# Performance work log

Measured on AMD Instinct MI355X. Metric: run time of the kernel, lower is better.

The kernel has to match this reference:

```python
import jax, jax.numpy as jnp
import numpy as np

B, C, T, H = 2, 1024, 2048, 16
D = C // H  # head dim = 64
SCALE = 1.0 / np.sqrt(D)
NEG_INF = jnp.float32(-1e30)


def setup_inputs() -> dict:
    key = jax.random.key(0)
    ks = jax.random.split(key, 10)
    x = jax.random.normal(ks[0], (B, C, T), dtype=jnp.float32)
    mask = jax.random.randint(ks[1], (B, 1, T), 0, 2).astype(bool)
    mask = mask.at[:, :, 0].set(True)  # avoid all-masked rows -> NaN softmax
    w = 1.0 / np.sqrt(C)
    Wq = jax.random.normal(ks[2], (C, C), dtype=jnp.float32) * w
    bq = jax.random.normal(ks[3], (C,), dtype=jnp.float32) * 0.01
    Wk = jax.random.normal(ks[4], (C, C), dtype=jnp.float32) * w
    bk = jax.random.normal(ks[5], (C,), dtype=jnp.float32) * 0.01
    Wv = jax.random.normal(ks[6], (C, C), dtype=jnp.float32) * w
    bv = jax.random.normal(ks[7], (C,), dtype=jnp.float32) * 0.01
    Wp = jax.random.normal(ks[8], (C, C), dtype=jnp.float32) * w
    bp = jax.random.normal(ks[9], (C,), dtype=jnp.float32) * 0.01
    return {"x": x, "mask": mask, "Wq": Wq, "bq": bq, "Wk": Wk, "bk": bk,
            "Wv": Wv, "bv": bv, "Wp": Wp, "bp": bp}


def _proj(W, b, x):
    # Conv1d with kernel_size=1: per-timestep linear on [B, C, T]
    return jnp.einsum('oc,bct->bot', W, x) + b[:, None]


def _heads(y):
    # [B, C, T] -> [B, H, T, D]
    return y.reshape(B, H, D, T).transpose(0, 1, 3, 2)


def reference(x, mask, Wq, bq, Wk, bk, Wv, bv, Wp, bp):
    q = _heads(_proj(Wq, bq, x))  # [B,H,T,D]
    k = _heads(_proj(Wk, bk, x))
    v = _heads(_proj(Wv, bv, x))
    att = jnp.einsum('bhqd,bhkd->bhqk', q * SCALE, k)  # [B,H,T,T]
    att = jnp.where(mask[:, :, None, :], att, NEG_INF)  # mask keys
    att = jax.nn.softmax(att, axis=-1)
    vm = v * mask[:, :, :, None].astype(v.dtype)  # zero masked values
    out = jnp.einsum('bhqk,bhkd->bhqd', att, vm)  # [B,H,T,D]
    out = out.transpose(0, 1, 3, 2).reshape(B, C, T)
    out = _proj(Wp, bp, out) * mask.astype(x.dtype)  # [B,C,T]
    return (out, mask)
```

## Files before the change

kernel.cpp:

```cpp
#include <hip/hip_runtime.h>
#include <hip/hip_bf16.h>
#include <math.h>

#define BB 2
#define CC 1024
#define TT 2048
#define HH 16
#define DD 64

using short8   = __attribute__((ext_vector_type(8))) short;
using floatx4  = __attribute__((ext_vector_type(4))) float;
using floatx16 = __attribute__((ext_vector_type(16))) float;
using uint2v   = __attribute__((ext_vector_type(2))) unsigned int;
typedef unsigned short ushort_t;

#define MFMA(a, b, c) __builtin_amdgcn_mfma_f32_16x16x32_bf16((a), (b), (c), 0, 0, 0)
#define MFMA32(a, b, c) __builtin_amdgcn_mfma_f32_32x32x16_bf16((a), (b), (c), 0, 0, 0)

#define QSC 0.18033688011112042f

#define PMAGIC   8404857.0f
#define PZERO_BF 0.97265625f

__device__ __forceinline__ ushort_t f2bf(float f) {
    unsigned int u = __float_as_uint(f);
    u += 0x7FFFu + ((u >> 16) & 1u);
    return (ushort_t)(u >> 16);
}
__device__ __forceinline__ float bf2f(ushort_t h) {
    return __uint_as_float(((unsigned int)h) << 16);
}
__device__ __forceinline__ ushort_t f2bf_t(float f) {
    return (ushort_t)(__float_as_uint(f) >> 16);
}
__device__ __forceinline__ unsigned int packtrunc(float a, float b) {
    return __builtin_amdgcn_perm(__float_as_uint(b), __float_as_uint(a),
                                 0x07060302u);
}
__device__ __forceinline__ unsigned int pack2bf_exp(float s0, float s1) {
    float f0 = fmaf(s0, 128.0f, PMAGIC);
    float f1 = fmaf(s1, 128.0f, PMAGIC);
    return __builtin_amdgcn_perm(__float_as_uint(f1), __float_as_uint(f0),
                                 0x05040100u);
}
__device__ __forceinline__ void load_lds16(const void* g, void* s) {
    __builtin_amdgcn_global_load_lds(
        (const __attribute__((address_space(1))) void*)g,
        (__attribute__((address_space(3))) void*)s, 16, 0, 0);
}

static constexpr size_t B0       = 65536;
static constexpr size_t XT_OFF   = B0;
static constexpr size_t WQKV_OFF = XT_OFF   + 8388608;
static constexpr size_t WP_OFF   = WQKV_OFF + 6291456;
static constexpr size_t Q_OFF    = WP_OFF   + 2097152;
static constexpr size_t K_OFF    = Q_OFF    + 8388608;
static constexpr size_t V_OFF    = K_OFF    + 8388608;
static constexpr size_t OP_OFF   = V_OFF    + 8388608;
static constexpr size_t ML_OFF   = OP_OFF   + 16777216;

__global__ __launch_bounds__(256) void prep_kernel(
    const float* __restrict__ x, const float* __restrict__ Wq,
    const float* __restrict__ Wk, const float* __restrict__ Wv,
    const float* __restrict__ Wp, const unsigned int* __restrict__ mraw,
    ushort_t* __restrict__ XT, ushort_t* __restrict__ WQKV,
    ushort_t* __restrict__ WP, float* __restrict__ maskf,
    int* __restrict__ nmcnt, float* __restrict__ out_tail) {
    __shared__ float tile[64][65];
    const int bid = blockIdx.x;
    const int tid = threadIdx.x;
    if (bid < 4096) {
        const int idx = bid * 256 + tid;
        if (idx < 786432) {
            int row = idx >> 8;
            int qc  = idx & 255;
            const float* src = row < 1024 ? Wq : (row < 2048 ? Wk : Wv);
            float4 v = *(const float4*)&src[(size_t)(row & 1023) * CC + qc * 4];
            ushort4 pk; pk.x = f2bf(v.x); pk.y = f2bf(v.y);
            pk.z = f2bf(v.z); pk.w = f2bf(v.w);
            *(ushort4*)&WQKV[(size_t)idx * 4] = pk;
        } else {
            int j = idx - 786432;
            float4 v = *(const float4*)&Wp[(size_t)j * 4];
            ushort4 pk; pk.x = f2bf(v.x); pk.y = f2bf(v.y);
            pk.z = f2bf(v.z); pk.w = f2bf(v.w);
            *(ushort4*)&WP[(size_t)j * 4] = pk;
        }
    } else if (bid < 5120) {
        const int xb = bid - 4096;
        const int t0 = (xb & 31) * 64, c0 = ((xb >> 5) & 15) * 64, b = xb >> 9;
        const int tc = tid & 15, tr = tid >> 4;
        #pragma unroll
        for (int p = 0; p < 4; p++) {
            int cl = tr + p * 16;
            float4 v = *(const float4*)&x[((size_t)b * CC + c0 + cl) * TT + t0 + tc * 4];
            tile[cl][tc * 4 + 0] = v.x; tile[cl][tc * 4 + 1] = v.y;
            tile[cl][tc * 4 + 2] = v.z; tile[cl][tc * 4 + 3] = v.w;
        }
        __syncthreads();
        #pragma unroll
        for (int p = 0; p < 4; p++) {
            int tl = tr + p * 16;
            ushort4 pk;
            pk.x = f2bf(tile[tc * 4 + 0][tl]);
            pk.y = f2bf(tile[tc * 4 + 1][tl]);
            pk.z = f2bf(tile[tc * 4 + 2][tl]);
            pk.w = f2bf(tile[tc * 4 + 3][tl]);
            *(ushort4*)&XT[((size_t)b * TT + t0 + tl) * CC + c0 + tc * 4] = pk;
        }
    } else {
        __shared__ int ev_bf16, ev_bool, cnt;
        const int mb = bid - 5120;
        if (tid == 0) { ev_bf16 = 0; ev_bool = 0; cnt = 0; }
        __syncthreads();
        for (int i = tid; i < 1024; i += 256) {
            unsigned int w = mraw[i];
            if ((w & 0xFFFFu) == 0x3F80u) atomicOr(&ev_bf16, 1);
            if ((w & 0xFFFFFF00u) != 0u && w != 0x3F800000u) atomicOr(&ev_bool, 1);
        }
        __syncthreads();
        const int mode = ev_bf16 ? 2 : (ev_bool ? 1 : 0);
        const int e = mb * 256 + tid;
        bool on;
        if (mode == 2)      on = ((const ushort_t*)mraw)[e] != 0;
        else if (mode == 1) on = ((const unsigned char*)mraw)[e] != 0;
        else                on = mraw[e] != 0;
        maskf[e]    = on ? 1.0f : 0.0f;
        out_tail[e] = on ? 1.0f : 0.0f;
        if (!on) atomicAdd(&cnt, 1);
        __syncthreads();
        if (tid == 0) nmcnt[mb] = cnt;
    }
}

__global__ __launch_bounds__(256) void gemm_qkv_kernel(
    const ushort_t* __restrict__ Wqkv, const float* __restrict__ bq,
    const float* __restrict__ bk, const float* __restrict__ bv,
    const ushort_t* __restrict__ XT, const float* __restrict__ maskf,
    ushort_t* __restrict__ Qo, ushort_t* __restrict__ Ko,
    ushort_t* __restrict__ Vo) {
    __shared__ ushort_t As[128][32];
    __shared__ ushort_t Bs[128][32];
    __shared__ float biasS[128];

    const int b = blockIdx.z;
    const int m0 = blockIdx.y * 128;
    const int n0 = blockIdx.x * 128;
    const int tid = threadIdx.x;
    const int lane = tid & 63;
    const int w = tid >> 6;
    const int wm = (w & 1) * 64, wn = (w >> 1) * 64;
    const int la = lane & 15, lg = lane >> 4;
    const int region = m0 >> 10;

    const float* bsrc = region == 0 ? (bq + m0)
                      : (region == 1 ? (bk + m0 - 1024) : (bv + m0 - 2048));
    if (tid < 128) biasS[tid] = bsrc[tid];

    float csc[4];
    #pragma unroll
    for (int nt = 0; nt < 4; nt++) {
        const int t = n0 + wn + nt * 16 + la;
        csc[nt] = (region == 0) ? QSC : maskf[b * TT + t];
    }

    floatx4 zero4 = {0.f, 0.f, 0.f, 0.f};
    floatx4 acc[4][4];
    #pragma unroll
    for (int mt = 0; mt < 4; mt++)
        #pragma unroll
        for (int nt = 0; nt < 4; nt++) acc[mt][nt] = zero4;

    const ushort_t* Abase = Wqkv + (size_t)m0 * CC;
    const ushort_t* Bbase = XT + ((size_t)b * TT + n0) * CC;
    const int rl = lane >> 2;
    const int cl = (lane & 3) * 8;

    for (int k0 = 0; k0 < CC; k0 += 32) {
        #pragma unroll
        for (int c = 0; c < 2; c++) {
            int row = w * 32 + c * 16;
            load_lds16(Abase + (size_t)(row + rl) * CC + k0 + cl, &As[row][0]);
            load_lds16(Bbase + (size_t)(row + rl) * CC + k0 + cl, &Bs[row][0]);
        }
        __syncthreads();
        short8 af[4], bf[4];
        #pragma unroll
        for (int mt = 0; mt < 4; mt++)
            af[mt] = *(const short8*)&As[wm + mt * 16 + la][lg * 8];
        #pragma unroll
        for (int nt = 0; nt < 4; nt++)
            bf[nt] = *(const short8*)&Bs[wn + nt * 16 + la][lg * 8];
        #pragma unroll
        for (int mt = 0; mt < 4; mt++)
            #pragma unroll
            for (int nt = 0; nt < 4; nt++)
                acc[mt][nt] = MFMA(af[mt], bf[nt], acc[mt][nt]);
        __syncthreads();
    }

    #pragma unroll
    for (int mt = 0; mt < 4; mt++) {
        const int lm = wm + mt * 16 + lg * 4;
        const int gm = m0 + lm;
        #pragma unroll
        for (int nt = 0; nt < 4; nt++) {
            const int t = n0 + wn + nt * 16 + la;
            const float sc = csc[nt];
            float v0 = (acc[mt][nt][0] + biasS[lm + 0]) * sc;
            float v1 = (acc[mt][nt][1] + biasS[lm + 1]) * sc;
            float v2 = (acc[mt][nt][2] + biasS[lm + 2]) * sc;
            float v3 = (acc[mt][nt][3] + biasS[lm + 3]) * sc;
            if (region < 2) {
                int mq = gm & 1023;
                int hh = mq >> 6, db = mq & 63;
                ushort_t* dst = (region == 0 ? Qo : Ko)
                              + (((size_t)b * HH + hh) * TT + t) * DD + db;
                uint2 pk;
                pk.x = packtrunc(v0, v1);
                pk.y = packtrunc(v2, v3);
                *(uint2*)dst = pk;
            } else {
                int c = gm & 1023;
                Vo[((size_t)b * CC + c + 0) * TT + t] = f2bf_t(v0);
                Vo[((size_t)b * CC + c + 1) * TT + t] = f2bf_t(v1);
                Vo[((size_t)b * CC + c + 2) * TT + t] = f2bf_t(v2);
                Vo[((size_t)b * CC + c + 3) * TT + t] = f2bf_t(v3);
            }
        }
    }
}

__global__ __launch_bounds__(256, 4) void attn_kernel(
    const ushort_t* __restrict__ Qg, const ushort_t* __restrict__ Kg,
    const ushort_t* __restrict__ Vg, const int* __restrict__ nmcnt,
    ushort_t* __restrict__ Opart, float* __restrict__ lbuf) {
    __shared__ __align__(16) char ldsbuf[32768];

    const unsigned int bid = blockIdx.x;
    const unsigned int xcd = bid & 7u;
    const unsigned int rr  = bid >> 3;
    const unsigned int x   = rr & 15u;
    const unsigned int j   = rr >> 4;
    const unsigned int g   = (j << 3) | xcd;
    const int hh  = (int)(g & 15u);
    const int z   = (int)(g >> 4);
    const int sp  = z & 1, b = z >> 1;
    const int t0  = (int)x * 128;

    const int j0base = sp * (TT / 2);
    const int tid  = threadIdx.x;
    const int lane = tid & 63;
    const int w    = tid >> 6;
    const int ln31 = lane & 31;
    const int h    = lane >> 5;
    const size_t qkbase = ((size_t)b * HH + hh) * TT * DD;
    const size_t vbase  = ((size_t)b * CC + hh * DD) * TT;

    const int tq = t0 + w * 32 + ln31;
    short8 qreg[4];
    {
        const ushort_t* qp = Qg + qkbase + (size_t)tq * DD + h * 8;
        #pragma unroll
        for (int kc = 0; kc < 4; kc++)
            qreg[kc] = *(const short8*)(qp + kc * 16);
    }

    const int i3   = lane >> 3;
    const int swzb = (((lane & 7) + 8 - i3) & 7) << 4;
    const char* ks0 = (const char*)(Kg + qkbase + (size_t)(j0base + 16 * w + i3) * DD) + swzb;
    const char* vs0 = (const char*)(Vg + vbase + (size_t)(16 * w + i3) * TT + j0base) + swzb;
    char* kd = ldsbuf + 2 * w * 1024;
    char* vd = ldsbuf + 16384 + 2 * w * 1024;

    int ka[4];
    #pragma unroll
    for (int kc = 0; kc < 4; kc++)
        ka[kc] = ln31 * 128 + (((kc * 2 + h + ln31) & 7) << 4);

    floatx16 zero16 = {0.f,0.f,0.f,0.f,0.f,0.f,0.f,0.f,
                       0.f,0.f,0.f,0.f,0.f,0.f,0.f,0.f};
    floatx16 oacc[2];
    oacc[0] = zero16; oacc[1] = zero16;
    floatx16 lacc = zero16;
    short8 ones8;
    #pragma unroll
    for (int i = 0; i < 8; i++) ones8[i] = (short)0x3F80;

    load_lds16(ks0,          kd);
    load_lds16(ks0 + 1024,   kd + 1024);
    load_lds16(vs0,          vd);
    load_lds16(vs0 + 32768,  vd + 1024);
    ks0 += 8192; vs0 += 128;
    __syncthreads();

    #pragma unroll 2
    for (int kt = 0; kt < 16; kt++) {
        const int pp = (kt & 1) * 8192;
        const int pn = 8192 - pp;
        if (kt < 15) {
            load_lds16(ks0,         kd + pn);
            load_lds16(ks0 + 1024,  kd + pn + 1024);
            load_lds16(vs0,         vd + pn);
            load_lds16(vs0 + 32768, vd + pn + 1024);
            ks0 += 8192; vs0 += 128;
        }

        floatx16 sacc[2];
        sacc[0] = zero16; sacc[1] = zero16;
        __builtin_amdgcn_s_setprio(1);
        #pragma unroll
        for (int kc = 0; kc < 4; kc++) {
            short8 kf0 = *(const short8*)(ldsbuf + ka[kc] + pp);
            short8 kf1 = *(const short8*)(ldsbuf + ka[kc] + pp + 4096);
            sacc[0] = MFMA32(kf0, qreg[kc], sacc[0]);
            sacc[1] = MFMA32(kf1, qreg[kc], sacc[1]);
        }
        __builtin_amdgcn_s_setprio(0);

        unsigned int pd[16];
        #pragma unroll
        for (int mt = 0; mt < 2; mt++)
            #pragma unroll
            for (int g2 = 0; g2 < 4; g2++) {
                pd[mt * 8 + g2 * 2 + 0] =
                    pack2bf_exp(sacc[mt][g2 * 4 + 0], sacc[mt][g2 * 4 + 1]);
                pd[mt * 8 + g2 * 2 + 1] =
                    pack2bf_exp(sacc[mt][g2 * 4 + 2], sacc[mt][g2 * 4 + 3]);
            }

        __builtin_amdgcn_s_setprio(1);
        #pragma unroll
        for (int kc = 0; kc < 4; kc++) {
            const int base = (kc >> 1) * 8 + (kc & 1) * 4;
            uint2v r02 = __builtin_amdgcn_permlane32_swap(
                pd[base + 0], pd[base + 2], false, false);
            uint2v r13 = __builtin_amdgcn_permlane32_swap(
                pd[base + 1], pd[base + 3], false, false);
            int4 fi;
            fi.x = (int)r02[0];
            fi.y = (int)r13[0];
            fi.z = (int)r02[1];
            fi.w = (int)r13[1];
            short8 pf = *(short8*)&fi;
            lacc = MFMA32(ones8, pf, lacc);
            short8 vf0 = *(const short8*)(ldsbuf + ka[kc] + pp + 16384);
            short8 vf1 = *(const short8*)(ldsbuf + ka[kc] + pp + 16384 + 4096);
            oacc[0] = MFMA32(vf0, pf, oacc[0]);
            oacc[1] = MFMA32(vf1, pf, oacc[1]);
        }
        __builtin_amdgcn_s_setprio(0);

        if (kt < 15) __syncthreads();
    }

    float lsum = lacc[0];
    {
        const int r4 = (b * 2 + sp) * 4;
        int nm = nmcnt[r4] + nmcnt[r4 + 1] + nmcnt[r4 + 2] + nmcnt[r4 + 3];
        lsum -= (float)nm * PZERO_BF;
    }

    const float inv = lsum > 0.0f ? 1.0f / lsum : 0.0f;
    ushort_t* OP = Opart + (size_t)sp * ((size_t)BB * TT * CC)
                 + ((size_t)b * TT + tq) * CC + hh * 64;
    #pragma unroll
    for (int mt = 0; mt < 2; mt++)
        #pragma unroll
        for (int g2 = 0; g2 < 4; g2++) {
            int db = mt * 32 + g2 * 8 + h * 4;
            ushort4 pk;
            pk.x = f2bf(oacc[mt][g2 * 4 + 0] * inv);
            pk.y = f2bf(oacc[mt][g2 * 4 + 1] * inv);
            pk.z = f2bf(oacc[mt][g2 * 4 + 2] * inv);
            pk.w = f2bf(oacc[mt][g2 * 4 + 3] * inv);
            *(ushort4*)&OP[db] = pk;
        }
    if (h == 0)
        lbuf[(((size_t)sp * BB + b) * HH + hh) * TT + tq] = lsum;
}

__global__ __launch_bounds__(256) void combine_kernel(
    const ushort_t* __restrict__ Opart, const float* __restrict__ lbuf,
    ushort_t* __restrict__ OT) {
    const size_t idx = ((size_t)blockIdx.x * 256 + threadIdx.x) * 8;
    const int c0 = (int)(idx & (CC - 1));
    const int t  = (int)((idx >> 10) & (TT - 1));
    const int b  = (int)(idx >> 21);
    const int hh = c0 >> 6;
    const float l0 = lbuf[(((size_t)0 * BB + b) * HH + hh) * TT + t];
    const float l1 = lbuf[(((size_t)1 * BB + b) * HH + hh) * TT + t];
    const float sum = l0 + l1;
    const float ws = sum > 0.0f ? 1.0f / sum : 0.0f;
    const float w0 = l0 * ws, w1 = l1 * ws;
    const ushort_t* P0 = Opart + idx;
    const ushort_t* P1 = Opart + (size_t)BB * TT * CC + idx;
    ushort4 a0 = *(const ushort4*)(P0);
    ushort4 a1 = *(const ushort4*)(P0 + 4);
    ushort4 b0 = *(const ushort4*)(P1);
    ushort4 b1 = *(const ushort4*)(P1 + 4);
    ushort4 o0, o1;
    o0.x = f2bf(w0 * bf2f(a0.x) + w1 * bf2f(b0.x));
    o0.y = f2bf(w0 * bf2f(a0.y) + w1 * bf2f(b0.y));
    o0.z = f2bf(w0 * bf2f(a0.z) + w1 * bf2f(b0.z));
    o0.w = f2bf(w0 * bf2f(a0.w) + w1 * bf2f(b0.w));
    o1.x = f2bf(w0 * bf2f(a1.x) + w1 * bf2f(b1.x));
    o1.y = f2bf(w0 * bf2f(a1.y) + w1 * bf2f(b1.y));
    o1.z = f2bf(w0 * bf2f(a1.z) + w1 * bf2f(b1.z));
    o1.w = f2bf(w0 * bf2f(a1.w) + w1 * bf2f(b1.w));
    *(ushort4*)&OT[idx]     = o0;
    *(ushort4*)&OT[idx + 4] = o1;
}

__global__ __launch_bounds__(256) void gemm_out_kernel(
    const ushort_t* __restrict__ WP, const ushort_t* __restrict__ OT,
    const float* __restrict__ bp, const float* __restrict__ maskf,
    float* __restrict__ out) {
    __shared__ ushort_t As[64][32];
    __shared__ ushort_t Bs[128][32];
    __shared__ float biasS[64];

    const int b = blockIdx.z;
    const int m0 = blockIdx.y * 64;
    const int n0 = blockIdx.x * 128;
    const int tid = threadIdx.x;
    const int lane = tid & 63;
    const int w = tid >> 6;
    const int wm = (w & 1) * 32, wn = (w >> 1) * 64;
    const int la = lane & 15, lg = lane >> 4;

    if (tid < 64) biasS[tid] = bp[m0 + tid];

    floatx4 zero4 = {0.f, 0.f, 0.f, 0.f};
    floatx4 acc[2][4];
    #pragma unroll
    for (int mt = 0; mt < 2; mt++)
        #pragma unroll
        for (int nt = 0; nt < 4; nt++) acc[mt][nt] = zero4;

    const int rl = lane >> 2;
    const int cl = (lane & 3) * 8;
    const ushort_t* Bbase = OT + ((size_t)b * TT + n0) * CC;

    for (int k0 = 0; k0 < CC; k0 += 32) {
        {
            int row = w * 16;
            load_lds16(WP + (size_t)(m0 + row + rl) * CC + k0 + cl, &As[row][0]);
        }
        #pragma unroll
        for (int c = 0; c < 2; c++) {
            int row = w * 32 + c * 16;
            load_lds16(Bbase + (size_t)(row + rl) * CC + k0 + cl, &Bs[row][0]);
        }
        __syncthreads();
        short8 af[2], bf[4];
        #pragma unroll
        for (int mt = 0; mt < 2; mt++)
            af[mt] = *(const short8*)&As[wm + mt * 16 + la][lg * 8];
        #pragma unroll
        for (int nt = 0; nt < 4; nt++)
            bf[nt] = *(const short8*)&Bs[wn + nt * 16 + la][lg * 8];
        #pragma unroll
        for (int mt = 0; mt < 2; mt++)
            #pragma unroll
            for (int nt = 0; nt < 4; nt++)
                acc[mt][nt] = MFMA(af[mt], bf[nt], acc[mt][nt]);
        __syncthreads();
    }

    #pragma unroll
    for (int mt = 0; mt < 2; mt++) {
        const int lm = wm + mt * 16 + lg * 4;
        #pragma unroll
        for (int nt = 0; nt < 4; nt++) {
            const int t = n0 + wn + nt * 16 + la;
            const float mk = maskf[b * TT + t];
            #pragma unroll
            for (int r = 0; r < 4; r++)
                out[((size_t)b * CC + m0 + lm + r) * TT + t] =
                    (acc[mt][nt][r] + biasS[lm + r]) * mk;
        }
    }
}

extern "C" void kernel_launch(void* const* d_in, const int* in_sizes, int n_in,
                              void* d_out, int out_size, void* d_ws,
                              size_t ws_size, hipStream_t stream) {
    const float* x    = (const float*)d_in[0];
    const void*  mask = d_in[1];
    const float* Wq   = (const float*)d_in[2];
    const float* bq   = (const float*)d_in[3];
    const float* Wk   = (const float*)d_in[4];
    const float* bk   = (const float*)d_in[5];
    const float* Wv   = (const float*)d_in[6];
    const float* bv   = (const float*)d_in[7];
    const float* Wp   = (const float*)d_in[8];
    const float* bp   = (const float*)d_in[9];

    float* out  = (float*)d_out;
    float* wsf  = (float*)d_ws;
    int* nmcnt  = (int*)d_ws + 16;
    float* maskf = wsf + 1024;
    char* wsb = (char*)d_ws;
    ushort_t* XT    = (ushort_t*)(wsb + XT_OFF);
    ushort_t* WQKV  = (ushort_t*)(wsb + WQKV_OFF);
    ushort_t* WPb   = (ushort_t*)(wsb + WP_OFF);
    ushort_t* Qb    = (ushort_t*)(wsb + Q_OFF);
    ushort_t* Kb    = (ushort_t*)(wsb + K_OFF);
    ushort_t* Vb    = (ushort_t*)(wsb + V_OFF);
    ushort_t* Opart = (ushort_t*)(wsb + OP_OFF);
    float*    lbuf  = (float*)(wsb + ML_OFF);

    prep_kernel<<<5136, 256, 0, stream>>>(x, Wq, Wk, Wv, Wp,
                                          (const unsigned int*)mask, XT, WQKV,
                                          WPb, maskf, nmcnt,
                                          out + (size_t)BB * CC * TT);

    gemm_qkv_kernel<<<dim3(TT / 128, 3 * CC / 128, BB), 256, 0, stream>>>(
        WQKV, bq, bk, bv, XT, maskf, Qb, Kb, Vb);

    attn_kernel<<<dim3(1024), 256, 0, stream>>>(
        Qb, Kb, Vb, nmcnt, Opart, lbuf);

    combine_kernel<<<2048, 256, 0, stream>>>(Opart, lbuf, XT);

    gemm_out_kernel<<<dim3(TT / 128, CC / 64, BB), 256, 0, stream>>>(
        WPb, XT, bp, maskf, out);
}
```

Measured before the change: 192.0 us.

## Process two 32-query tiles per wave in attention, halving block threads

The attention kernel now uses 128-thread blocks where each wave handles two 32-row query tiles (A and B) that share each K/V fragment read from LDS. Each wave therefore does twice the MFMA work per LDS fragment load, and the cooperative K/V tile staging is spread over two waves with four loads each. The cost is roughly double the accumulator and probability registers per wave, which raises register pressure. Launch bounds change to (128, 2), which can reduce occupancy and latency hiding.

```diff
diff --git a/kernel.cpp b/kernel.cpp
--- a/kernel.cpp
+++ b/kernel.cpp
@@ -231,7 +231,7 @@
     }
 }
 
-__global__ __launch_bounds__(256, 4) void attn_kernel(
+__global__ __launch_bounds__(128, 2) void attn_kernel(
     const ushort_t* __restrict__ Qg, const ushort_t* __restrict__ Kg,
     const ushort_t* __restrict__ Vg, const int* __restrict__ nmcnt,
     ushort_t* __restrict__ Opart, float* __restrict__ lbuf) {
@@ -257,21 +257,26 @@
     const size_t qkbase = ((size_t)b * HH + hh) * TT * DD;
     const size_t vbase  = ((size_t)b * CC + hh * DD) * TT;
 
-    const int tq = t0 + w * 32 + ln31;
-    short8 qreg[4];
+    const int tqA = t0 + w * 64 + ln31;
+    short8 qrA[4], qrB[4];
     {
-        const ushort_t* qp = Qg + qkbase + (size_t)tq * DD + h * 8;
-        #pragma unroll
-        for (int kc = 0; kc < 4; kc++)
-            qreg[kc] = *(const short8*)(qp + kc * 16);
+        const ushort_t* qpA = Qg + qkbase + (size_t)tqA * DD + h * 8;
+        const ushort_t* qpB = qpA + 32 * DD;
+        #pragma unroll
+        for (int kc = 0; kc < 4; kc++) {
+            qrA[kc] = *(const short8*)(qpA + kc * 16);
+            qrB[kc] = *(const short8*)(qpB + kc * 16);
+        }
     }
 
     const int i3   = lane >> 3;
     const int swzb = (((lane & 7) + 8 - i3) & 7) << 4;
-    const char* ks0 = (const char*)(Kg + qkbase + (size_t)(j0base + 16 * w + i3) * DD) + swzb;
-    const char* vs0 = (const char*)(Vg + vbase + (size_t)(16 * w + i3) * TT + j0base) + swzb;
-    char* kd = ldsbuf + 2 * w * 1024;
-    char* vd = ldsbuf + 16384 + 2 * w * 1024;
+    const char* ksrc = (const char*)(Kg + qkbase)
+                     + (((size_t)(j0base + w * 32 + i3)) << 7) + swzb;
+    const char* vsrc = (const char*)(Vg + vbase)
+                     + ((size_t)(w * 32 + i3) * TT + j0base) * 2 + swzb;
+    char* kdst = ldsbuf + w * 4096;
+    char* vdst = ldsbuf + 16384 + w * 4096;
 
     int ka[4];
     #pragma unroll
@@ -280,18 +285,19 @@
 
     floatx16 zero16 = {0.f,0.f,0.f,0.f,0.f,0.f,0.f,0.f,
                        0.f,0.f,0.f,0.f,0.f,0.f,0.f,0.f};
-    floatx16 oacc[2];
-    oacc[0] = zero16; oacc[1] = zero16;
-    floatx16 lacc = zero16;
+    floatx16 oaccA[2], oaccB[2];
+    oaccA[0] = zero16; oaccA[1] = zero16;
+    oaccB[0] = zero16; oaccB[1] = zero16;
+    floatx16 laccA = zero16, laccB = zero16;
     short8 ones8;
     #pragma unroll
     for (int i = 0; i < 8; i++) ones8[i] = (short)0x3F80;
 
-    load_lds16(ks0,          kd);
-    load_lds16(ks0 + 1024,   kd + 1024);
-    load_lds16(vs0,          vd);
-    load_lds16(vs0 + 32768,  vd + 1024);
-    ks0 += 8192; vs0 += 128;
+    #pragma unroll
+    for (int gg = 0; gg < 4; gg++) {
+        load_lds16(ksrc + gg * 1024, kdst + gg * 1024);
+        load_lds16(vsrc + (size_t)gg * 32768, vdst + gg * 1024);
+    }
     __syncthreads();
 
     #pragma unroll 2
@@ -299,85 +305,114 @@
         const int pp = (kt & 1) * 8192;
         const int pn = 8192 - pp;
         if (kt < 15) {
-            load_lds16(ks0,         kd + pn);
-            load_lds16(ks0 + 1024,  kd + pn + 1024);
-            load_lds16(vs0,         vd + pn);
-            load_lds16(vs0 + 32768, vd + pn + 1024);
-            ks0 += 8192; vs0 += 128;
-        }
-
-        floatx16 sacc[2];
-        sacc[0] = zero16; sacc[1] = zero16;
+            const size_t ko = (size_t)(kt + 1) * 8192;
+            const size_t vo = (size_t)(kt + 1) * 128;
+            #pragma unroll
+            for (int gg = 0; gg < 4; gg++) {
+                load_lds16(ksrc + ko + gg * 1024, kdst + pn + gg * 1024);
+                load_lds16(vsrc + vo + (size_t)gg * 32768, vdst + pn + gg * 1024);
+            }
+        }
+
+        floatx16 sA0 = zero16, sA1 = zero16, sB0 = zero16, sB1 = zero16;
         __builtin_amdgcn_s_setprio(1);
         #pragma unroll
         for (int kc = 0; kc < 4; kc++) {
             short8 kf0 = *(const short8*)(ldsbuf + ka[kc] + pp);
             short8 kf1 = *(const short8*)(ldsbuf + ka[kc] + pp + 4096);
-            sacc[0] = MFMA32(kf0, qreg[kc], sacc[0]);
-            sacc[1] = MFMA32(kf1, qreg[kc], sacc[1]);
+            sA0 = MFMA32(kf0, qrA[kc], sA0);
+            sA1 = MFMA32(kf1, qrA[kc], sA1);
+            sB0 = MFMA32(kf0, qrB[kc], sB0);
+            sB1 = MFMA32(kf1, qrB[kc], sB1);
         }
         __builtin_amdgcn_s_setprio(0);
 
-        unsigned int pd[16];
-        #pragma unroll
-        for (int mt = 0; mt < 2; mt++)
-            #pragma unroll
-            for (int g2 = 0; g2 < 4; g2++) {
-                pd[mt * 8 + g2 * 2 + 0] =
-                    pack2bf_exp(sacc[mt][g2 * 4 + 0], sacc[mt][g2 * 4 + 1]);
-                pd[mt * 8 + g2 * 2 + 1] =
-                    pack2bf_exp(sacc[mt][g2 * 4 + 2], sacc[mt][g2 * 4 + 3]);
-            }
+        unsigned int pdA[16], pdB[16];
+        #pragma unroll
+        for (int g2 = 0; g2 < 4; g2++) {
+            pdA[g2 * 2 + 0] = pack2bf_exp(sA0[g2 * 4 + 0], sA0[g2 * 4 + 1]);
+            pdA[g2 * 2 + 1] = pack2bf_exp(sA0[g2 * 4 + 2], sA0[g2 * 4 + 3]);
+            pdA[8 + g2 * 2 + 0] = pack2bf_exp(sA1[g2 * 4 + 0], sA1[g2 * 4 + 1]);
+            pdA[8 + g2 * 2 + 1] = pack2bf_exp(sA1[g2 * 4 + 2], sA1[g2 * 4 + 3]);
+            pdB[g2 * 2 + 0] = pack2bf_exp(sB0[g2 * 4 + 0], sB0[g2 * 4 + 1]);
+            pdB[g2 * 2 + 1] = pack2bf_exp(sB0[g2 * 4 + 2], sB0[g2 * 4 + 3]);
+            pdB[8 + g2 * 2 + 0] = pack2bf_exp(sB1[g2 * 4 + 0], sB1[g2 * 4 + 1]);
+            pdB[8 + g2 * 2 + 1] = pack2bf_exp(sB1[g2 * 4 + 2], sB1[g2 * 4 + 3]);
+        }
 
         __builtin_amdgcn_s_setprio(1);
         #pragma unroll
         for (int kc = 0; kc < 4; kc++) {
             const int base = (kc >> 1) * 8 + (kc & 1) * 4;
-            uint2v r02 = __builtin_amdgcn_permlane32_swap(
-                pd[base + 0], pd[base + 2], false, false);
-            uint2v r13 = __builtin_amdgcn_permlane32_swap(
-                pd[base + 1], pd[base + 3], false, false);
-            int4 fi;
-            fi.x = (int)r02[0];
-            fi.y = (int)r13[0];
-            fi.z = (int)r02[1];
-            fi.w = (int)r13[1];
-            short8 pf = *(short8*)&fi;
-            lacc = MFMA32(ones8, pf, lacc);
             short8 vf0 = *(const short8*)(ldsbuf + ka[kc] + pp + 16384);
             short8 vf1 = *(const short8*)(ldsbuf + ka[kc] + pp + 16384 + 4096);
-            oacc[0] = MFMA32(vf0, pf, oacc[0]);
-            oacc[1] = MFMA32(vf1, pf, oacc[1]);
+            {
+                uint2v r02 = __builtin_amdgcn_permlane32_swap(
+                    pdA[base + 0], pdA[base + 2], false, false);
+                uint2v r13 = __builtin_amdgcn_permlane32_swap(
+                    pdA[base + 1], pdA[base + 3], false, false);
+                int4 fi;
+                fi.x = (int)r02[0]; fi.y = (int)r13[0];
+                fi.z = (int)r02[1]; fi.w = (int)r13[1];
+                short8 pf = *(short8*)&fi;
+                laccA = MFMA32(ones8, pf, laccA);
+                oaccA[0] = MFMA32(vf0, pf, oaccA[0]);
+                oaccA[1] = MFMA32(vf1, pf, oaccA[1]);
+            }
+            {
+                uint2v r02 = __builtin_amdgcn_permlane32_swap(
+                    pdB[base + 0], pdB[base + 2], false, false);
+                uint2v r13 = __builtin_amdgcn_permlane32_swap(
+                    pdB[base + 1], pdB[base + 3], false, false);
+                int4 fi;
+                fi.x = (int)r02[0]; fi.y = (int)r13[0];
+                fi.z = (int)r02[1]; fi.w = (int)r13[1];
+                short8 pf = *(short8*)&fi;
+                laccB = MFMA32(ones8, pf, laccB);
+                oaccB[0] = MFMA32(vf0, pf, oaccB[0]);
+                oaccB[1] = MFMA32(vf1, pf, oaccB[1]);
+            }
         }
         __builtin_amdgcn_s_setprio(0);
 
         if (kt < 15) __syncthreads();
     }
 
-    float lsum = lacc[0];
+    float lsA = laccA[0], lsB = laccB[0];
     {
         const int r4 = (b * 2 + sp) * 4;
         int nm = nmcnt[r4] + nmcnt[r4 + 1] + nmcnt[r4 + 2] + nmcnt[r4 + 3];
-        lsum -= (float)nm * PZERO_BF;
-    }
-
-    const float inv = lsum > 0.0f ? 1.0f / lsum : 0.0f;
-    ushort_t* OP = Opart + (size_t)sp * ((size_t)BB * TT * CC)
-                 + ((size_t)b * TT + tq) * CC + hh * 64;
+        float corr = (float)nm * PZERO_BF;
+        lsA -= corr; lsB -= corr;
+    }
+
+    const float invA = lsA > 0.0f ? 1.0f / lsA : 0.0f;
+    const float invB = lsB > 0.0f ? 1.0f / lsB : 0.0f;
+    ushort_t* OPA = Opart + (size_t)sp * ((size_t)BB * TT * CC)
+                  + ((size_t)b * TT + tqA) * CC + hh * 64;
+    ushort_t* OPB = OPA + (size_t)32 * CC;
     #pragma unroll
     for (int mt = 0; mt < 2; mt++)
         #pragma unroll
         for (int g2 = 0; g2 < 4; g2++) {
             int db = mt * 32 + g2 * 8 + h * 4;
             ushort4 pk;
-            pk.x = f2bf(oacc[mt][g2 * 4 + 0] * inv);
-            pk.y = f2bf(oacc[mt][g2 * 4 + 1] * inv);
-            pk.z = f2bf(oacc[mt][g2 * 4 + 2] * inv);
-            pk.w = f2bf(oacc[mt][g2 * 4 + 3] * inv);
-            *(ushort4*)&OP[db] = pk;
-        }
-    if (h == 0)
-        lbuf[(((size_t)sp * BB + b) * HH + hh) * TT + tq] = lsum;
+            pk.x = f2bf(oaccA[mt][g2 * 4 + 0] * invA);
+            pk.y = f2bf(oaccA[mt][g2 * 4 + 1] * invA);
+            pk.z = f2bf(oaccA[mt][g2 * 4 + 2] * invA);
+            pk.w = f2bf(oaccA[mt][g2 * 4 + 3] * invA);
+            *(ushort4*)&OPA[db] = pk;
+            pk.x = f2bf(oaccB[mt][g2 * 4 + 0] * invB);
+            pk.y = f2bf(oaccB[mt][g2 * 4 + 1] * invB);
+            pk.z = f2bf(oaccB[mt][g2 * 4 + 2] * invB);
+            pk.w = f2bf(oaccB[mt][g2 * 4 + 3] * invB);
+            *(ushort4*)&OPB[db] = pk;
+        }
+    if (h == 0) {
+        float* lp = lbuf + (((size_t)sp * BB + b) * HH + hh) * TT + tqA;
+        lp[0]  = lsA;
+        lp[32] = lsB;
+    }
 }
 
 __global__ __launch_bounds__(256) void combine_kernel(
@@ -519,7 +554,7 @@
     gemm_qkv_kernel<<<dim3(TT / 128, 3 * CC / 128, BB), 256, 0, stream>>>(
         WQKV, bq, bk, bv, XT, maskf, Qb, Kb, Vb);
 
-    attn_kernel<<<dim3(1024), 256, 0, stream>>>(
+    attn_kernel<<<dim3(1024), 128, 0, stream>>>(
         Qb, Kb, Vb, nmcnt, Opart, lbuf);
 
     combine_kernel<<<2048, 256, 0, stream>>>(Opart, lbuf, XT);
```

After: 193.1 us. No clear change (+0.6%).

## Shrink attention blocks to two waves and single-buffer V in LDS

Applied to the files above, without the earlier changes.

The attention kernel now launches 2048 blocks of 128 threads, each covering 64 query rows instead of 128. LDS per block drops from 32 KB to 24 KB because V is single-buffered while K stays double-buffered. V is loaded at the start of each iteration, and an extra barrier after the QK^T/exp stage orders the V load against its reads. The goal is more resident blocks and better latency hiding. The cost is an additional sync per tile, V loads that are less overlapped with compute, and each block loading K/V for half as many queries, which doubles total K/V traffic.

```diff
diff --git a/kernel.cpp b/kernel.cpp
--- a/kernel.cpp
+++ b/kernel.cpp
@@ -231,22 +231,22 @@
     }
 }
 
-__global__ __launch_bounds__(256, 4) void attn_kernel(
+__global__ __launch_bounds__(128, 4) void attn_kernel(
     const ushort_t* __restrict__ Qg, const ushort_t* __restrict__ Kg,
     const ushort_t* __restrict__ Vg, const int* __restrict__ nmcnt,
     ushort_t* __restrict__ Opart, float* __restrict__ lbuf) {
-    __shared__ __align__(16) char ldsbuf[32768];
+    __shared__ __align__(16) char ldsbuf[24576];
 
     const unsigned int bid = blockIdx.x;
     const unsigned int xcd = bid & 7u;
     const unsigned int rr  = bid >> 3;
-    const unsigned int x   = rr & 15u;
-    const unsigned int j   = rr >> 4;
+    const unsigned int x   = rr & 31u;
+    const unsigned int j   = rr >> 5;
     const unsigned int g   = (j << 3) | xcd;
     const int hh  = (int)(g & 15u);
     const int z   = (int)(g >> 4);
     const int sp  = z & 1, b = z >> 1;
-    const int t0  = (int)x * 128;
+    const int t0  = (int)x * 64;
 
     const int j0base = sp * (TT / 2);
     const int tid  = threadIdx.x;
@@ -268,10 +268,12 @@
 
     const int i3   = lane >> 3;
     const int swzb = (((lane & 7) + 8 - i3) & 7) << 4;
-    const char* ks0 = (const char*)(Kg + qkbase + (size_t)(j0base + 16 * w + i3) * DD) + swzb;
-    const char* vs0 = (const char*)(Vg + vbase + (size_t)(16 * w + i3) * TT + j0base) + swzb;
-    char* kd = ldsbuf + 2 * w * 1024;
-    char* vd = ldsbuf + 16384 + 2 * w * 1024;
+    const char* ksrc = (const char*)(Kg + qkbase)
+                     + (((size_t)(j0base + w * 32 + i3)) << 7) + swzb;
+    const char* vsrc = (const char*)(Vg + vbase)
+                     + ((size_t)(w * 32 + i3) * TT + j0base) * 2 + swzb;
+    char* kdst = ldsbuf + w * 4096;
+    char* vdst = ldsbuf + 16384 + w * 4096;
 
     int ka[4];
     #pragma unroll
@@ -287,23 +289,28 @@
     #pragma unroll
     for (int i = 0; i < 8; i++) ones8[i] = (short)0x3F80;
 
-    load_lds16(ks0,          kd);
-    load_lds16(ks0 + 1024,   kd + 1024);
-    load_lds16(vs0,          vd);
-    load_lds16(vs0 + 32768,  vd + 1024);
-    ks0 += 8192; vs0 += 128;
+    #pragma unroll
+    for (int gg = 0; gg < 4; gg++) {
+        load_lds16(ksrc + gg * 1024, kdst + gg * 1024);
+        load_lds16(vsrc + (size_t)gg * 32768, vdst + gg * 1024);
+    }
     __syncthreads();
 
     #pragma unroll 2
     for (int kt = 0; kt < 16; kt++) {
         const int pp = (kt & 1) * 8192;
-        const int pn = 8192 - pp;
+        if (kt > 0) {
+            const size_t vo = (size_t)kt * 128;
+            #pragma unroll
+            for (int gg = 0; gg < 4; gg++)
+                load_lds16(vsrc + vo + (size_t)gg * 32768, vdst + gg * 1024);
+        }
         if (kt < 15) {
-            load_lds16(ks0,         kd + pn);
-            load_lds16(ks0 + 1024,  kd + pn + 1024);
-            load_lds16(vs0,         vd + pn);
-            load_lds16(vs0 + 32768, vd + pn + 1024);
-            ks0 += 8192; vs0 += 128;
+            const size_t ko = (size_t)(kt + 1) * 8192;
+            char* kd = kdst + (8192 - pp);
+            #pragma unroll
+            for (int gg = 0; gg < 4; gg++)
+                load_lds16(ksrc + ko + gg * 1024, kd + gg * 1024);
         }
 
         floatx16 sacc[2];
@@ -328,6 +335,8 @@
                 pd[mt * 8 + g2 * 2 + 1] =
                     pack2bf_exp(sacc[mt][g2 * 4 + 2], sacc[mt][g2 * 4 + 3]);
             }
+
+        __syncthreads();
 
         __builtin_amdgcn_s_setprio(1);
         #pragma unroll
@@ -344,8 +353,8 @@
             fi.w = (int)r13[1];
             short8 pf = *(short8*)&fi;
             lacc = MFMA32(ones8, pf, lacc);
-            short8 vf0 = *(const short8*)(ldsbuf + ka[kc] + pp + 16384);
-            short8 vf1 = *(const short8*)(ldsbuf + ka[kc] + pp + 16384 + 4096);
+            short8 vf0 = *(const short8*)(ldsbuf + ka[kc] + 16384);
+            short8 vf1 = *(const short8*)(ldsbuf + ka[kc] + 16384 + 4096);
             oacc[0] = MFMA32(vf0, pf, oacc[0]);
             oacc[1] = MFMA32(vf1, pf, oacc[1]);
         }
@@ -519,7 +528,7 @@
     gemm_qkv_kernel<<<dim3(TT / 128, 3 * CC / 128, BB), 256, 0, stream>>>(
         WQKV, bq, bk, bv, XT, maskf, Qb, Kb, Vb);
 
-    attn_kernel<<<dim3(1024), 256, 0, stream>>>(
+    attn_kernel<<<dim3(2048), 128, 0, stream>>>(
         Qb, Kb, Vb, nmcnt, Opart, lbuf);
 
     combine_kernel<<<2048, 256, 0, stream>>>(Opart, lbuf, XT);
```

New measurement: 206.2 us. 7.4% more time.

## Double-buffer LDS tiles in QKV and output projection GEMMs

Applied to the files above, without the earlier changes.

Both projection GEMMs now use two LDS buffers for the A and B tiles. The next K-slice's global-to-LDS loads are issued before the MFMAs on the current slice, so each iteration needs one barrier instead of two and memory latency can overlap with compute. The MFMA block is also wrapped in s_setprio to raise wave priority during matrix math. This doubles LDS use per block, which may reduce occupancy, and correctness depends on the asynchronous LDS loads being complete by the next barrier.

```diff
diff --git a/kernel.cpp b/kernel.cpp
--- a/kernel.cpp
+++ b/kernel.cpp
@@ -139,8 +139,8 @@
     const ushort_t* __restrict__ XT, const float* __restrict__ maskf,
     ushort_t* __restrict__ Qo, ushort_t* __restrict__ Ko,
     ushort_t* __restrict__ Vo) {
-    __shared__ ushort_t As[128][32];
-    __shared__ ushort_t Bs[128][32];
+    __shared__ ushort_t As[2][128][32];
+    __shared__ ushort_t Bs[2][128][32];
     __shared__ float biasS[128];
 
     const int b = blockIdx.z;
@@ -176,27 +176,42 @@
     const int rl = lane >> 2;
     const int cl = (lane & 3) * 8;
 
-    for (int k0 = 0; k0 < CC; k0 += 32) {
-        #pragma unroll
-        for (int c = 0; c < 2; c++) {
-            int row = w * 32 + c * 16;
-            load_lds16(Abase + (size_t)(row + rl) * CC + k0 + cl, &As[row][0]);
-            load_lds16(Bbase + (size_t)(row + rl) * CC + k0 + cl, &Bs[row][0]);
-        }
-        __syncthreads();
+    #pragma unroll
+    for (int c = 0; c < 2; c++) {
+        int row = w * 32 + c * 16;
+        load_lds16(Abase + (size_t)(row + rl) * CC + cl, &As[0][row][0]);
+        load_lds16(Bbase + (size_t)(row + rl) * CC + cl, &Bs[0][row][0]);
+    }
+    __syncthreads();
+
+    for (int kt = 0; kt < 32; kt++) {
+        const int cur = kt & 1;
+        if (kt < 31) {
+            const int k0n = (kt + 1) * 32;
+            #pragma unroll
+            for (int c = 0; c < 2; c++) {
+                int row = w * 32 + c * 16;
+                load_lds16(Abase + (size_t)(row + rl) * CC + k0n + cl,
+                           &As[cur ^ 1][row][0]);
+                load_lds16(Bbase + (size_t)(row + rl) * CC + k0n + cl,
+                           &Bs[cur ^ 1][row][0]);
+            }
+        }
         short8 af[4], bf[4];
         #pragma unroll
         for (int mt = 0; mt < 4; mt++)
-            af[mt] = *(const short8*)&As[wm + mt * 16 + la][lg * 8];
+            af[mt] = *(const short8*)&As[cur][wm + mt * 16 + la][lg * 8];
         #pragma unroll
         for (int nt = 0; nt < 4; nt++)
-            bf[nt] = *(const short8*)&Bs[wn + nt * 16 + la][lg * 8];
+            bf[nt] = *(const short8*)&Bs[cur][wn + nt * 16 + la][lg * 8];
+        __builtin_amdgcn_s_setprio(1);
         #pragma unroll
         for (int mt = 0; mt < 4; mt++)
             #pragma unroll
             for (int nt = 0; nt < 4; nt++)
                 acc[mt][nt] = MFMA(af[mt], bf[nt], acc[mt][nt]);
-        __syncthreads();
+        __builtin_amdgcn_s_setprio(0);
+        if (kt < 31) __syncthreads();
     }
 
     #pragma unroll
@@ -416,8 +431,8 @@
     const ushort_t* __restrict__ WP, const ushort_t* __restrict__ OT,
     const float* __restrict__ bp, const float* __restrict__ maskf,
     float* __restrict__ out) {
-    __shared__ ushort_t As[64][32];
-    __shared__ ushort_t Bs[128][32];
+    __shared__ ushort_t As[2][64][32];
+    __shared__ ushort_t Bs[2][128][32];
     __shared__ float biasS[64];
 
     const int b = blockIdx.z;
@@ -442,30 +457,48 @@
     const int cl = (lane & 3) * 8;
     const ushort_t* Bbase = OT + ((size_t)b * TT + n0) * CC;
 
-    for (int k0 = 0; k0 < CC; k0 += 32) {
-        {
-            int row = w * 16;
-            load_lds16(WP + (size_t)(m0 + row + rl) * CC + k0 + cl, &As[row][0]);
-        }
-        #pragma unroll
-        for (int c = 0; c < 2; c++) {
-            int row = w * 32 + c * 16;
-            load_lds16(Bbase + (size_t)(row + rl) * CC + k0 + cl, &Bs[row][0]);
-        }
-        __syncthreads();
+    {
+        int row = w * 16;
+        load_lds16(WP + (size_t)(m0 + row + rl) * CC + cl, &As[0][row][0]);
+    }
+    #pragma unroll
+    for (int c = 0; c < 2; c++) {
+        int row = w * 32 + c * 16;
+        load_lds16(Bbase + (size_t)(row + rl) * CC + cl, &Bs[0][row][0]);
+    }
+    __syncthreads();
+
+    for (int kt = 0; kt < 32; kt++) {
+        const int cur = kt & 1;
+        if (kt < 31) {
+            const int k0n = (kt + 1) * 32;
+            {
+                int row = w * 16;
+                load_lds16(WP + (size_t)(m0 + row + rl) * CC + k0n + cl,
+                           &As[cur ^ 1][row][0]);
+            }
+            #pragma unroll
+            for (int c = 0; c < 2; c++) {
+                int row = w * 32 + c * 16;
+                load_lds16(Bbase + (size_t)(row + rl) * CC + k0n + cl,
+                           &Bs[cur ^ 1][row][0]);
+            }
+        }
         short8 af[2], bf[4];
         #pragma unroll
         for (int mt = 0; mt < 2; mt++)
-            af[mt] = *(const short8*)&As[wm + mt * 16 + la][lg * 8];
+            af[mt] = *(const short8*)&As[cur][wm + mt * 16 + la][lg * 8];
         #pragma unroll
         for (int nt = 0; nt < 4; nt++)
-            bf[nt] = *(const short8*)&Bs[wn + nt * 16 + la][lg * 8];
+            bf[nt] = *(const short8*)&Bs[cur][wn + nt * 16 + la][lg * 8];
+        __builtin_amdgcn_s_setprio(1);
         #pragma unroll
         for (int mt = 0; mt < 2; mt++)
             #pragma unroll
             for (int nt = 0; nt < 4; nt++)
                 acc[mt][nt] = MFMA(af[mt], bf[nt], acc[mt][nt]);
-        __syncthreads();
+        __builtin_amdgcn_s_setprio(0);
+        if (kt < 31) __syncthreads();
     }
 
     #pragma unroll
```

After: 194.6 us. No clear change (+1.4%).
